# Performance work log

Hardware: AMD Instinct MI355X
Metric: run time of the kernel (lower is better)

Reference implementation:

```python
import jax, jax.numpy as jnp
import numpy as np

N = 50000   # nodes
E = 800000  # edges per layer
D = 128     # feature dim
H = 256     # mlp hidden
O = 3       # output dim


def setup_inputs() -> dict:
    key = jax.random.key(0)
    ks = jax.random.split(key, 16)
    def lin(k, fan_out, fan_in):
        s = 1.0 / np.sqrt(fan_in)
        kw, kb = jax.random.split(k)
        return (jax.random.uniform(kw, (fan_out, fan_in), jnp.float32, -s, s),
                jax.random.uniform(kb, (fan_out,), jnp.float32, -s, s))
    x = jax.random.normal(ks[0], (N, D), jnp.float32)
    edge_idx0 = jax.random.randint(ks[1], (2, E), 0, N, dtype=jnp.int64)
    edge_idx1 = jax.random.randint(ks[2], (2, E), 0, N, dtype=jnp.int64)
    Wl1, bl1 = lin(ks[3], D, D)   # SAGE layer1: lin_l (aggregated neighbors, with bias)
    Wr1, _ = lin(ks[4], D, D)     # SAGE layer1: lin_r (root, no bias)
    Wl2, bl2 = lin(ks[5], D, D)
    Wr2, _ = lin(ks[6], D, D)
    Ws, bs = lin(ks[7], D, D)     # skip_fc
    W1, b1 = lin(ks[8], H, D)     # mlp hidden
    W2, b2 = lin(ks[9], O, H)     # mlp out
    return dict(x=x, edge_idx0=edge_idx0, edge_idx1=edge_idx1,
                Wl1=Wl1, bl1=bl1, Wr1=Wr1, Wl2=Wl2, bl2=bl2, Wr2=Wr2,
                Ws=Ws, bs=bs, W1=W1, b1=b1, W2=W2, b2=b2)


def _sage(x, ei, Wl, bl, Wr):
    # PyG SAGEConv with mean aggregation: out = lin_l(mean_j x_j) + lin_r(x_i)
    src, dst = ei[0], ei[1]
    agg = jax.ops.segment_sum(x[src], dst, num_segments=N)          # [N, D] gather-scatter
    cnt = jax.ops.segment_sum(jnp.ones((ei.shape[1],), x.dtype), dst, num_segments=N)
    agg = agg / jnp.maximum(cnt, 1.0)[:, None]
    return agg @ Wl.T + bl + x @ Wr.T


def reference(x, edge_idx0, edge_idx1, Wl1, bl1, Wr1, Wl2, bl2, Wr2,
              Ws, bs, W1, b1, W2, b2):
    inp = x
    h = _sage(x, edge_idx0, Wl1, bl1, Wr1)
    h = _sage(h, edge_idx1, Wl2, bl2, Wr2)
    h = h + (inp @ Ws.T + bs)            # skip connection
    h = jax.nn.relu(h @ W1.T + b1)       # MLP head
    return h @ W2.T + b2                  # [N, 3]
```

## Files before the change

kernel.cpp:

```cpp
#include <hip/hip_runtime.h>
#include <hip/hip_bf16.h>


#define DD 128
#define SB 8
#define CH 4096
typedef unsigned short u16;
typedef __attribute__((ext_vector_type(8))) short short8;
typedef __attribute__((ext_vector_type(4))) float f32x4;

__device__ inline u16 f2bf(float f) {
    __hip_bfloat16 h = __float2bfloat16(f);
    u16 u;
    __builtin_memcpy(&u, &h, 2);
    return u;
}
__device__ inline unsigned pack2(float lo, float hi) {
    return (unsigned)f2bf(lo) | ((unsigned)f2bf(hi) << 16);
}
__device__ inline float bf_lo(unsigned u) { union { unsigned x; float f; } c; c.x = u << 16; return c.f; }
__device__ inline float bf_hi(unsigned u) { union { unsigned x; float f; } c; c.x = u & 0xffff0000u; return c.f; }

struct CastJobs {
    const float4* src[6];
    uint2* dst[6];
    int qstart[7];
};
__global__ __launch_bounds__(256) void cast_kernel(CastJobs jb) {
    int q = blockIdx.x * 256 + threadIdx.x;
    if (q >= jb.qstart[6]) return;
    int i = 0;
#pragma unroll
    for (int k = 1; k < 6; ++k) if (q >= jb.qstart[k]) i = k;
    int local = q - jb.qstart[i];
    float4 v = jb.src[i][local];
    jb.dst[i][local] = make_uint2(pack2(v.x, v.y), pack2(v.z, v.w));
}

__global__ __launch_bounds__(256) void hist1_kernel(const int* __restrict__ dst0, int* __restrict__ h0,
                                                    const int* __restrict__ dst1, int* __restrict__ h1,
                                                    int e0, int e1, int nb, int P) {
    int arr = blockIdx.y;
    const int* dst = arr ? dst1 : dst0;
    int* hist = arr ? h1 : h0;
    int e = arr ? e1 : e0;
    __shared__ int h[256];
    int t = threadIdx.x;
    h[t] = 0;
    __syncthreads();
    int base = blockIdx.x * CH;
    int hi = min(base + CH, e);
    for (int i = base + t; i < hi; i += 256) atomicAdd(&h[dst[i] >> SB], 1);
    __syncthreads();
    if (t < nb) hist[t * P + blockIdx.x] = h[t];
}

__global__ __launch_bounds__(256) void rowsum_kernel(const int* __restrict__ h0, int* __restrict__ bs0,
                                                     const int* __restrict__ h1, int* __restrict__ bs1,
                                                     int P) {
    int arr = blockIdx.y;
    const int* hist = arr ? h1 : h0;
    int* bs = arr ? bs1 : bs0;
    int b = blockIdx.x;
    __shared__ int s[256];
    int t = threadIdx.x;
    s[t] = (t < P) ? hist[b * P + t] : 0;
    __syncthreads();
    for (int off = 128; off; off >>= 1) {
        if (t < off) s[t] += s[t + off];
        __syncthreads();
    }
    if (t == 0) bs[b] = s[0];
}

__global__ __launch_bounds__(256) void bscan_kernel(const int* __restrict__ bs0, int* __restrict__ bb0, int* __restrict__ rp0, int e0,
                                                    const int* __restrict__ bs1, int* __restrict__ bb1, int* __restrict__ rp1, int e1,
                                                    int nb, int n) {
    int arr = blockIdx.x;
    const int* bsum = arr ? bs1 : bs0;
    int* bb = arr ? bb1 : bb0;
    int* rp = arr ? rp1 : rp0;
    int E = arr ? e1 : e0;
    __shared__ int s[256];
    int t = threadIdx.x;
    int v = (t < nb) ? bsum[t] : 0;
    s[t] = v;
    __syncthreads();
    for (int off = 1; off < 256; off <<= 1) {
        int u = (t >= off) ? s[t - off] : 0;
        __syncthreads();
        s[t] += u;
        __syncthreads();
    }
    if (t < nb) bb[t] = s[t] - v;
    if (t == 0) { bb[nb] = E; rp[n] = E; }
}

__global__ __launch_bounds__(256) void offs_kernel(int* __restrict__ h0, const int* __restrict__ bb0,
                                                   int* __restrict__ h1, const int* __restrict__ bb1,
                                                   int P) {
    int arr = blockIdx.y;
    int* hist = arr ? h1 : h0;
    const int* bb = arr ? bb1 : bb0;
    int b = blockIdx.x;
    __shared__ int s[256];
    int t = threadIdx.x;
    int v = (t < P) ? hist[b * P + t] : 0;
    s[t] = v;
    __syncthreads();
    for (int off = 1; off < 256; off <<= 1) {
        int u = (t >= off) ? s[t - off] : 0;
        __syncthreads();
        s[t] += u;
        __syncthreads();
    }
    if (t < P) hist[b * P + t] = s[t] - v + bb[b];
}

__global__ __launch_bounds__(256) void scatter1_kernel(
    const int* __restrict__ src0, const int* __restrict__ dst0, const int* __restrict__ h0, unsigned* __restrict__ binned0,
    const int* __restrict__ src1, const int* __restrict__ dst1, const int* __restrict__ h1, unsigned* __restrict__ binned1,
    int e0, int e1, int nb, int P) {
    int arr = blockIdx.y;
    const int* src = arr ? src1 : src0;
    const int* dst = arr ? dst1 : dst0;
    const int* hist = arr ? h1 : h0;
    unsigned* binned = arr ? binned1 : binned0;
    int e = arr ? e1 : e0;
    int p = blockIdx.x;
    __shared__ int cnt[256];
    int t = threadIdx.x;
    if (t < nb) cnt[t] = hist[t * P + p];
    __syncthreads();
    int base = p * CH;
    int hi = min(base + CH, e);
    for (int i = base + t; i < hi; i += 256) {
        int d = dst[i];
        int pos = atomicAdd(&cnt[d >> SB], 1);
        binned[pos] = ((unsigned)d << 16) | (unsigned)src[i];
    }
}

__global__ __launch_bounds__(256) void place_kernel(
    const unsigned* __restrict__ binned0, const int* __restrict__ bb0, int* __restrict__ rp0, u16* __restrict__ csr0,
    const unsigned* __restrict__ binned1, const int* __restrict__ bb1, int* __restrict__ rp1, u16* __restrict__ csr1,
    int n, int nb) {
    int arr = blockIdx.y;
    const unsigned* binned = arr ? binned1 : binned0;
    const int* bb = arr ? bb1 : bb0;
    int* rp = arr ? rp1 : rp0;
    u16* csr = arr ? csr1 : csr0;
    int b = blockIdx.x;
    __shared__ int cnt[256];
    __shared__ int s[256];
    int t = threadIdx.x;
    int base = bb[b], end = bb[b + 1];
    cnt[t] = 0;
    __syncthreads();
    for (int i = base + t; i < end; i += 256)
        atomicAdd(&cnt[(binned[i] >> 16) & 255], 1);
    __syncthreads();
    int deg = cnt[t];
    s[t] = deg;
    __syncthreads();
    for (int off = 1; off < 256; off <<= 1) {
        int u = (t >= off) ? s[t - off] : 0;
        __syncthreads();
        s[t] += u;
        __syncthreads();
    }
    int gpos = base + s[t] - deg;
    int node = (b << SB) + t;
    if (node < n) rp[node] = gpos;
    cnt[t] = gpos;
    __syncthreads();
    for (int i = base + t; i < end; i += 256) {
        unsigned pk = binned[i];
        int ld = (pk >> 16) & 255;
        int pos = atomicAdd(&cnt[ld], 1);
        csr[pos] = (u16)(pk & 0xffffu);
    }
}

__global__ __launch_bounds__(256) void agg1_kernel(const u16* __restrict__ G1,
                                                   const u16* __restrict__ csr,
                                                   const int* __restrict__ rp,
                                                   const float* __restrict__ bl1,
                                                   u16* __restrict__ h1, int n) {
    int g = (blockIdx.x * 256 + threadIdx.x) >> 4;
    int lane = threadIdx.x & 15;
    if (g >= n) return;
    int start = rp[g], end = rp[g + 1];
    int d = end - start;
    const uint4* X4 = (const uint4*)G1;
    float acc[8] = {0.f, 0.f, 0.f, 0.f, 0.f, 0.f, 0.f, 0.f};
    int e = start;
    for (; e + 3 < end; e += 4) {
        int s0 = csr[e], s1 = csr[e + 1], s2 = csr[e + 2], s3 = csr[e + 3];
        uint4 v0 = X4[(size_t)s0 * 48 + lane];
        uint4 v1 = X4[(size_t)s1 * 48 + lane];
        uint4 v2 = X4[(size_t)s2 * 48 + lane];
        uint4 v3 = X4[(size_t)s3 * 48 + lane];
        acc[0] += (bf_lo(v0.x) + bf_lo(v1.x)) + (bf_lo(v2.x) + bf_lo(v3.x));
        acc[1] += (bf_hi(v0.x) + bf_hi(v1.x)) + (bf_hi(v2.x) + bf_hi(v3.x));
        acc[2] += (bf_lo(v0.y) + bf_lo(v1.y)) + (bf_lo(v2.y) + bf_lo(v3.y));
        acc[3] += (bf_hi(v0.y) + bf_hi(v1.y)) + (bf_hi(v2.y) + bf_hi(v3.y));
        acc[4] += (bf_lo(v0.z) + bf_lo(v1.z)) + (bf_lo(v2.z) + bf_lo(v3.z));
        acc[5] += (bf_hi(v0.z) + bf_hi(v1.z)) + (bf_hi(v2.z) + bf_hi(v3.z));
        acc[6] += (bf_lo(v0.w) + bf_lo(v1.w)) + (bf_lo(v2.w) + bf_lo(v3.w));
        acc[7] += (bf_hi(v0.w) + bf_hi(v1.w)) + (bf_hi(v2.w) + bf_hi(v3.w));
    }
    for (; e < end; ++e) {
        uint4 v0 = X4[(size_t)csr[e] * 48 + lane];
        acc[0] += bf_lo(v0.x); acc[1] += bf_hi(v0.x);
        acc[2] += bf_lo(v0.y); acc[3] += bf_hi(v0.y);
        acc[4] += bf_lo(v0.z); acc[5] += bf_hi(v0.z);
        acc[6] += bf_lo(v0.w); acc[7] += bf_hi(v0.w);
    }
    float sc = 1.0f / (float)max(d, 1);
    uint4 m = X4[(size_t)g * 48 + 16 + lane];
    const float4* bl = (const float4*)bl1;
    float4 ba = bl[lane * 2], bb = bl[lane * 2 + 1];
    uint4 r;
    r.x = pack2(acc[0] * sc + bf_lo(m.x) + ba.x, acc[1] * sc + bf_hi(m.x) + ba.y);
    r.y = pack2(acc[2] * sc + bf_lo(m.y) + ba.z, acc[3] * sc + bf_hi(m.y) + ba.w);
    r.z = pack2(acc[4] * sc + bf_lo(m.z) + bb.x, acc[5] * sc + bf_hi(m.z) + bb.y);
    r.w = pack2(acc[6] * sc + bf_lo(m.w) + bb.z, acc[7] * sc + bf_hi(m.w) + bb.w);
    ((uint4*)h1)[(size_t)g * 16 + lane] = r;
}

__global__ __launch_bounds__(256) void agg2_kernel(const u16* __restrict__ G2,
                                                   const u16* __restrict__ G1,
                                                   const u16* __restrict__ csr,
                                                   const int* __restrict__ rp,
                                                   const float* __restrict__ bl2,
                                                   const float* __restrict__ bs,
                                                   u16* __restrict__ h3, int n) {
    int g = (blockIdx.x * 256 + threadIdx.x) >> 4;
    int lane = threadIdx.x & 15;
    if (g >= n) return;
    int start = rp[g], end = rp[g + 1];
    int d = end - start;
    const uint4* X4 = (const uint4*)G2;
    float acc[8] = {0.f, 0.f, 0.f, 0.f, 0.f, 0.f, 0.f, 0.f};
    int e = start;
    for (; e + 3 < end; e += 4) {
        int s0 = csr[e], s1 = csr[e + 1], s2 = csr[e + 2], s3 = csr[e + 3];
        uint4 v0 = X4[(size_t)s0 * 32 + lane];
        uint4 v1 = X4[(size_t)s1 * 32 + lane];
        uint4 v2 = X4[(size_t)s2 * 32 + lane];
        uint4 v3 = X4[(size_t)s3 * 32 + lane];
        acc[0] += (bf_lo(v0.x) + bf_lo(v1.x)) + (bf_lo(v2.x) + bf_lo(v3.x));
        acc[1] += (bf_hi(v0.x) + bf_hi(v1.x)) + (bf_hi(v2.x) + bf_hi(v3.x));
        acc[2] += (bf_lo(v0.y) + bf_lo(v1.y)) + (bf_lo(v2.y) + bf_lo(v3.y));
        acc[3] += (bf_hi(v0.y) + bf_hi(v1.y)) + (bf_hi(v2.y) + bf_hi(v3.y));
        acc[4] += (bf_lo(v0.z) + bf_lo(v1.z)) + (bf_lo(v2.z) + bf_lo(v3.z));
        acc[5] += (bf_hi(v0.z) + bf_hi(v1.z)) + (bf_hi(v2.z) + bf_hi(v3.z));
        acc[6] += (bf_lo(v0.w) + bf_lo(v1.w)) + (bf_lo(v2.w) + bf_lo(v3.w));
        acc[7] += (bf_hi(v0.w) + bf_hi(v1.w)) + (bf_hi(v2.w) + bf_hi(v3.w));
    }
    for (; e < end; ++e) {
        uint4 v0 = X4[(size_t)csr[e] * 32 + lane];
        acc[0] += bf_lo(v0.x); acc[1] += bf_hi(v0.x);
        acc[2] += bf_lo(v0.y); acc[3] += bf_hi(v0.y);
        acc[4] += bf_lo(v0.z); acc[5] += bf_hi(v0.z);
        acc[6] += bf_lo(v0.w); acc[7] += bf_hi(v0.w);
    }
    float sc = 1.0f / (float)max(d, 1);
    uint4 m2 = X4[(size_t)g * 32 + 16 + lane];
    uint4 m1 = ((const uint4*)G1)[(size_t)g * 48 + 32 + lane];
    const float4* c2 = (const float4*)bl2;
    const float4* cs = (const float4*)bs;
    float4 ba = c2[lane * 2], bb = c2[lane * 2 + 1];
    float4 sa = cs[lane * 2], sb = cs[lane * 2 + 1];
    uint4 r;
    r.x = pack2(acc[0] * sc + bf_lo(m2.x) + bf_lo(m1.x) + ba.x + sa.x,
                acc[1] * sc + bf_hi(m2.x) + bf_hi(m1.x) + ba.y + sa.y);
    r.y = pack2(acc[2] * sc + bf_lo(m2.y) + bf_lo(m1.y) + ba.z + sa.z,
                acc[3] * sc + bf_hi(m2.y) + bf_hi(m1.y) + ba.w + sa.w);
    r.z = pack2(acc[4] * sc + bf_lo(m2.z) + bf_lo(m1.z) + bb.x + sb.x,
                acc[5] * sc + bf_hi(m2.z) + bf_hi(m1.z) + bb.y + sb.y);
    r.w = pack2(acc[6] * sc + bf_lo(m2.w) + bf_lo(m1.w) + bb.z + sb.z,
                acc[7] * sc + bf_hi(m2.w) + bf_hi(m1.w) + bb.w + sb.w);
    ((uint4*)h3)[(size_t)g * 16 + lane] = r;
}

template <bool F32A>
__global__ __launch_bounds__(256) void mfma_gemm(const void* __restrict__ Av,
                                                 const u16* __restrict__ W,
                                                 u16* __restrict__ C, int M, int NC) {
    __shared__ u16 Bs[32 * 512];
    const int t = threadIdx.x;
    const int colBase = blockIdx.y * 128;
#pragma unroll
    for (int i = 0; i < 8; ++i) {
        int id = t + 256 * i;
        int nrow = id >> 4, cc = id & 15;
        int f = ((nrow >> 4) << 2) | (cc >> 2);
        int dl = ((cc & 3) << 4) | (nrow & 15);
        *(uint4*)&Bs[(f * 64 + dl) * 8] = ((const uint4*)W)[(size_t)(colBase + nrow) * 16 + cc];
    }
    __syncthreads();
    const int w = t >> 6, lane = t & 63, r = lane & 15, half = lane >> 4;
    const int nTiles = M >> 4;
    const int nWaves = gridDim.x * 4;
    const u16* bB = &Bs[lane * 8];
    for (int tile = blockIdx.x * 4 + w; tile < nTiles; tile += nWaves) {
        int rowA = (tile << 4) + r;
        short8 af[4];
        if (F32A) {
            const float4* Arow = (const float4*)Av + (size_t)rowA * 32 + half * 2;
#pragma unroll
            for (int kk = 0; kk < 4; ++kk) {
                float4 a = Arow[kk * 8], b = Arow[kk * 8 + 1];
                uint4 v = make_uint4(pack2(a.x, a.y), pack2(a.z, a.w),
                                     pack2(b.x, b.y), pack2(b.z, b.w));
                af[kk] = *(short8*)&v;
            }
        } else {
            const uint4* Arow = (const uint4*)Av + (size_t)rowA * 16 + half;
#pragma unroll
            for (int kk = 0; kk < 4; ++kk) {
                uint4 v = Arow[kk * 4];
                af[kk] = *(short8*)&v;
            }
        }
        f32x4 acc[8];
#pragma unroll
        for (int i = 0; i < 8; ++i) acc[i] = (f32x4){0.f, 0.f, 0.f, 0.f};
#pragma unroll
        for (int kk = 0; kk < 4; ++kk)
#pragma unroll
            for (int ct = 0; ct < 8; ++ct) {
                short8 bf = *(const short8*)(bB + (ct * 4 + kk) * 512);
                acc[ct] = __builtin_amdgcn_mfma_f32_16x16x32_bf16(af[kk], bf, acc[ct], 0, 0, 0);
            }
#pragma unroll
        for (int ct = 0; ct < 8; ++ct) {
            int col = colBase + ct * 16 + r;
#pragma unroll
            for (int reg = 0; reg < 4; ++reg) {
                int row = (tile << 4) + half * 4 + reg;
                C[(size_t)row * NC + col] = f2bf(acc[ct][reg]);
            }
        }
    }
}

__global__ __launch_bounds__(256) void gemm_out_kernel(const u16* __restrict__ h3,
                                                       const u16* __restrict__ W1,
                                                       const float* __restrict__ b1,
                                                       const float* __restrict__ W2,
                                                       const float* __restrict__ b2,
                                                       float* __restrict__ out, int M) {
    __shared__ u16 Bs[64 * 512];
    __shared__ float w2s[3 * 256];
    __shared__ float b1s[256];
    const int t = threadIdx.x;
#pragma unroll
    for (int i = 0; i < 16; ++i) {
        int id = t + 256 * i;
        int nrow = id >> 4, cc = id & 15;
        int f = ((nrow >> 4) << 2) | (cc >> 2);
        int dl = ((cc & 3) << 4) | (nrow & 15);
        *(uint4*)&Bs[(f * 64 + dl) * 8] = ((const uint4*)W1)[(size_t)nrow * 16 + cc];
    }
    for (int i = t; i < 768; i += 256) w2s[i] = W2[i];
    b1s[t] = b1[t];
    __syncthreads();
    const int w = t >> 6, lane = t & 63, r = lane & 15, half = lane >> 4;
    const int nTiles = M >> 4;
    const int nWaves = gridDim.x * 4;
    const u16* bB = &Bs[lane * 8];
    float c0 = b2[0], c1 = b2[1], c2 = b2[2];
    for (int tile = blockIdx.x * 4 + w; tile < nTiles; tile += nWaves) {
        int rowA = (tile << 4) + r;
        const uint4* Arow = (const uint4*)h3 + (size_t)rowA * 16 + half;
        short8 af[4];
#pragma unroll
        for (int kk = 0; kk < 4; ++kk) {
            uint4 v = Arow[kk * 4];
            af[kk] = *(short8*)&v;
        }
        f32x4 acc[16];
#pragma unroll
        for (int i = 0; i < 16; ++i) acc[i] = (f32x4){0.f, 0.f, 0.f, 0.f};
#pragma unroll
        for (int kk = 0; kk < 4; ++kk)
#pragma unroll
            for (int ct = 0; ct < 16; ++ct) {
                short8 bf = *(const short8*)(bB + (ct * 4 + kk) * 512);
                acc[ct] = __builtin_amdgcn_mfma_f32_16x16x32_bf16(af[kk], bf, acc[ct], 0, 0, 0);
            }
        float p[4][3] = {{0.f, 0.f, 0.f}, {0.f, 0.f, 0.f}, {0.f, 0.f, 0.f}, {0.f, 0.f, 0.f}};
#pragma unroll
        for (int ct = 0; ct < 16; ++ct) {
            int col = ct * 16 + r;
            float bv = b1s[col];
            float w0 = w2s[col], w1 = w2s[256 + col], w2v = w2s[512 + col];
#pragma unroll
            for (int reg = 0; reg < 4; ++reg) {
                float h4 = fmaxf(acc[ct][reg] + bv, 0.f);
                p[reg][0] += h4 * w0;
                p[reg][1] += h4 * w1;
                p[reg][2] += h4 * w2v;
            }
        }
#pragma unroll
        for (int m = 1; m < 16; m <<= 1)
#pragma unroll
            for (int reg = 0; reg < 4; ++reg) {
                p[reg][0] += __shfl_xor(p[reg][0], m);
                p[reg][1] += __shfl_xor(p[reg][1], m);
                p[reg][2] += __shfl_xor(p[reg][2], m);
            }
        if (r == 0) {
#pragma unroll
            for (int reg = 0; reg < 4; ++reg) {
                int row = (tile << 4) + half * 4 + reg;
                out[(size_t)row * 3 + 0] = p[reg][0] + c0;
                out[(size_t)row * 3 + 1] = p[reg][1] + c1;
                out[(size_t)row * 3 + 2] = p[reg][2] + c2;
            }
        }
    }
}

extern "C" void kernel_launch(void* const* d_in, const int* in_sizes, int n_in,
                              void* d_out, int out_size, void* d_ws, size_t ws_size,
                              hipStream_t stream) {
    const float* x   = (const float*)d_in[0];
    const int*   ei0 = (const int*)d_in[1];
    const int*   ei1 = (const int*)d_in[2];
    const float* Wl1 = (const float*)d_in[3];
    const float* bl1 = (const float*)d_in[4];
    const float* Wr1 = (const float*)d_in[5];
    const float* Wl2 = (const float*)d_in[6];
    const float* bl2 = (const float*)d_in[7];
    const float* Wr2 = (const float*)d_in[8];
    const float* Wsk = (const float*)d_in[9];
    const float* bsk = (const float*)d_in[10];
    const float* W1  = (const float*)d_in[11];
    const float* b1  = (const float*)d_in[12];
    const float* W2  = (const float*)d_in[13];
    const float* b2  = (const float*)d_in[14];
    float* out = (float*)d_out;

    const int N  = in_sizes[0] / DD;
    const int E0 = in_sizes[1] / 2;
    const int E1 = in_sizes[2] / 2;
    const int H  = in_sizes[12];

    const int* src0 = ei0;      const int* dst0 = ei0 + E0;
    const int* src1 = ei1;      const int* dst1 = ei1 + E1;

    const int nb   = (N + 255) >> SB;
    const int Emax = (E0 > E1) ? E0 : E1;
    const int P    = (Emax + CH - 1) / CH;

    char* wp = (char*)d_ws;
    auto carve = [&](size_t bytes) { char* p = wp; wp += (bytes + 255) & ~(size_t)255; return p; };
    u16* G1   = (u16*)carve((size_t)N * 384 * 2);
    u16* G2   = (u16*)carve((size_t)N * 256 * 2);
    u16* h1h  = (u16*)carve((size_t)N * DD * 2);
    u16* h3h  = (u16*)carve((size_t)N * DD * 2);
    u16* wc1  = (u16*)carve((size_t)384 * DD * 2);
    u16* wc2  = (u16*)carve((size_t)256 * DD * 2);
    u16* w1h  = (u16*)carve((size_t)H * DD * 2);
    int* rp0  = (int*)carve((size_t)(N + 1) * 4);
    int* rp1  = (int*)carve((size_t)(N + 1) * 4);
    u16* csr0 = (u16*)carve((size_t)E0 * 2);
    u16* csr1 = (u16*)carve((size_t)E1 * 2);
    unsigned* binned0 = (unsigned*)carve((size_t)E0 * 4);
    unsigned* binned1 = (unsigned*)carve((size_t)E1 * 4);
    int* hist1_0 = (int*)carve((size_t)nb * P * 4);
    int* hist1_1 = (int*)carve((size_t)nb * P * 4);
    int* bsum0 = (int*)carve((size_t)nb * 4);
    int* bsum1 = (int*)carve((size_t)nb * 4);
    int* bb0 = (int*)carve((size_t)(nb + 1) * 4);
    int* bb1 = (int*)carve((size_t)(nb + 1) * 4);

    CastJobs jb;
    const float* srcs[6] = {Wl1, Wr1, Wsk, Wl2, Wr2, W1};
    u16* dsts[6] = {wc1, wc1 + 128 * DD, wc1 + 256 * DD, wc2, wc2 + 128 * DD, w1h};
    int  cnts[6] = {DD * DD, DD * DD, DD * DD, DD * DD, DD * DD, H * DD};
    int q = 0;
    for (int i = 0; i < 6; ++i) {
        jb.src[i] = (const float4*)srcs[i];
        jb.dst[i] = (uint2*)dsts[i];
        jb.qstart[i] = q;
        q += cnts[i] / 4;
    }
    jb.qstart[6] = q;

    const int gAgg = (N * 16 + 255) / 256;

    cast_kernel<<<(q + 255) / 256, 256, 0, stream>>>(jb);
    hist1_kernel<<<dim3(P, 2), 256, 0, stream>>>(dst0, hist1_0, dst1, hist1_1, E0, E1, nb, P);
    rowsum_kernel<<<dim3(nb, 2), 256, 0, stream>>>(hist1_0, bsum0, hist1_1, bsum1, P);
    bscan_kernel<<<2, 256, 0, stream>>>(bsum0, bb0, rp0, E0, bsum1, bb1, rp1, E1, nb, N);
    offs_kernel<<<dim3(nb, 2), 256, 0, stream>>>(hist1_0, bb0, hist1_1, bb1, P);
    scatter1_kernel<<<dim3(P, 2), 256, 0, stream>>>(src0, dst0, hist1_0, binned0,
                                                    src1, dst1, hist1_1, binned1, E0, E1, nb, P);
    place_kernel<<<dim3(nb, 2), 256, 0, stream>>>(binned0, bb0, rp0, csr0,
                                                  binned1, bb1, rp1, csr1, N, nb);

    mfma_gemm<true><<<dim3(320, 3), 256, 0, stream>>>(x, wc1, G1, N, 384);
    agg1_kernel<<<gAgg, 256, 0, stream>>>(G1, csr0, rp0, bl1, h1h, N);
    mfma_gemm<false><<<dim3(320, 2), 256, 0, stream>>>(h1h, wc2, G2, N, 256);
    agg2_kernel<<<gAgg, 256, 0, stream>>>(G2, G1, csr1, rp1, bl2, bsk, h3h, N);
    gemm_out_kernel<<<512, 256, 0, stream>>>(h3h, w1h, b1, W2, b2, out, N);
}
```

Baseline: 257.6 us.

## Fuse neighbor aggregation into following MFMA GEMMs and enlarge edge chunk size

The separate mean-aggregation kernels are removed. Aggregation for layer one now runs inside the layer-two GEMM, and aggregation for layer two inside the output MLP kernel. Each wave gathers the neighbor rows for its 16-row tile directly into MFMA A-fragments, which removes the h1/h3 intermediate writes and reads and two launches. The trade-off is that gathers become per-row and serialised across degree within a wave, with divergent loop lengths among the 16 rows of a tile, and only 512 blocks are launched. The edge chunk size for the binning passes is also doubled.

```diff
diff --git a/kernel.cpp b/kernel.cpp
--- a/kernel.cpp
+++ b/kernel.cpp
@@ -4,7 +4,7 @@
 
 #define DD 128
 #define SB 8
-#define CH 4096
+#define CH 8192
 typedef unsigned short u16;
 typedef __attribute__((ext_vector_type(8))) short short8;
 typedef __attribute__((ext_vector_type(4))) float f32x4;
@@ -182,109 +182,6 @@
     }
 }
 
-__global__ __launch_bounds__(256) void agg1_kernel(const u16* __restrict__ G1,
-                                                   const u16* __restrict__ csr,
-                                                   const int* __restrict__ rp,
-                                                   const float* __restrict__ bl1,
-                                                   u16* __restrict__ h1, int n) {
-    int g = (blockIdx.x * 256 + threadIdx.x) >> 4;
-    int lane = threadIdx.x & 15;
-    if (g >= n) return;
-    int start = rp[g], end = rp[g + 1];
-    int d = end - start;
-    const uint4* X4 = (const uint4*)G1;
-    float acc[8] = {0.f, 0.f, 0.f, 0.f, 0.f, 0.f, 0.f, 0.f};
-    int e = start;
-    for (; e + 3 < end; e += 4) {
-        int s0 = csr[e], s1 = csr[e + 1], s2 = csr[e + 2], s3 = csr[e + 3];
-        uint4 v0 = X4[(size_t)s0 * 48 + lane];
-        uint4 v1 = X4[(size_t)s1 * 48 + lane];
-        uint4 v2 = X4[(size_t)s2 * 48 + lane];
-        uint4 v3 = X4[(size_t)s3 * 48 + lane];
-        acc[0] += (bf_lo(v0.x) + bf_lo(v1.x)) + (bf_lo(v2.x) + bf_lo(v3.x));
-        acc[1] += (bf_hi(v0.x) + bf_hi(v1.x)) + (bf_hi(v2.x) + bf_hi(v3.x));
-        acc[2] += (bf_lo(v0.y) + bf_lo(v1.y)) + (bf_lo(v2.y) + bf_lo(v3.y));
-        acc[3] += (bf_hi(v0.y) + bf_hi(v1.y)) + (bf_hi(v2.y) + bf_hi(v3.y));
-        acc[4] += (bf_lo(v0.z) + bf_lo(v1.z)) + (bf_lo(v2.z) + bf_lo(v3.z));
-        acc[5] += (bf_hi(v0.z) + bf_hi(v1.z)) + (bf_hi(v2.z) + bf_hi(v3.z));
-        acc[6] += (bf_lo(v0.w) + bf_lo(v1.w)) + (bf_lo(v2.w) + bf_lo(v3.w));
-        acc[7] += (bf_hi(v0.w) + bf_hi(v1.w)) + (bf_hi(v2.w) + bf_hi(v3.w));
-    }
-    for (; e < end; ++e) {
-        uint4 v0 = X4[(size_t)csr[e] * 48 + lane];
-        acc[0] += bf_lo(v0.x); acc[1] += bf_hi(v0.x);
-        acc[2] += bf_lo(v0.y); acc[3] += bf_hi(v0.y);
-        acc[4] += bf_lo(v0.z); acc[5] += bf_hi(v0.z);
-        acc[6] += bf_lo(v0.w); acc[7] += bf_hi(v0.w);
-    }
-    float sc = 1.0f / (float)max(d, 1);
-    uint4 m = X4[(size_t)g * 48 + 16 + lane];
-    const float4* bl = (const float4*)bl1;
-    float4 ba = bl[lane * 2], bb = bl[lane * 2 + 1];
-    uint4 r;
-    r.x = pack2(acc[0] * sc + bf_lo(m.x) + ba.x, acc[1] * sc + bf_hi(m.x) + ba.y);
-    r.y = pack2(acc[2] * sc + bf_lo(m.y) + ba.z, acc[3] * sc + bf_hi(m.y) + ba.w);
-    r.z = pack2(acc[4] * sc + bf_lo(m.z) + bb.x, acc[5] * sc + bf_hi(m.z) + bb.y);
-    r.w = pack2(acc[6] * sc + bf_lo(m.w) + bb.z, acc[7] * sc + bf_hi(m.w) + bb.w);
-    ((uint4*)h1)[(size_t)g * 16 + lane] = r;
-}
-
-__global__ __launch_bounds__(256) void agg2_kernel(const u16* __restrict__ G2,
-                                                   const u16* __restrict__ G1,
-                                                   const u16* __restrict__ csr,
-                                                   const int* __restrict__ rp,
-                                                   const float* __restrict__ bl2,
-                                                   const float* __restrict__ bs,
-                                                   u16* __restrict__ h3, int n) {
-    int g = (blockIdx.x * 256 + threadIdx.x) >> 4;
-    int lane = threadIdx.x & 15;
-    if (g >= n) return;
-    int start = rp[g], end = rp[g + 1];
-    int d = end - start;
-    const uint4* X4 = (const uint4*)G2;
-    float acc[8] = {0.f, 0.f, 0.f, 0.f, 0.f, 0.f, 0.f, 0.f};
-    int e = start;
-    for (; e + 3 < end; e += 4) {
-        int s0 = csr[e], s1 = csr[e + 1], s2 = csr[e + 2], s3 = csr[e + 3];
-        uint4 v0 = X4[(size_t)s0 * 32 + lane];
-        uint4 v1 = X4[(size_t)s1 * 32 + lane];
-        uint4 v2 = X4[(size_t)s2 * 32 + lane];
-        uint4 v3 = X4[(size_t)s3 * 32 + lane];
-        acc[0] += (bf_lo(v0.x) + bf_lo(v1.x)) + (bf_lo(v2.x) + bf_lo(v3.x));
-        acc[1] += (bf_hi(v0.x) + bf_hi(v1.x)) + (bf_hi(v2.x) + bf_hi(v3.x));
-        acc[2] += (bf_lo(v0.y) + bf_lo(v1.y)) + (bf_lo(v2.y) + bf_lo(v3.y));
-        acc[3] += (bf_hi(v0.y) + bf_hi(v1.y)) + (bf_hi(v2.y) + bf_hi(v3.y));
-        acc[4] += (bf_lo(v0.z) + bf_lo(v1.z)) + (bf_lo(v2.z) + bf_lo(v3.z));
-        acc[5] += (bf_hi(v0.z) + bf_hi(v1.z)) + (bf_hi(v2.z) + bf_hi(v3.z));
-        acc[6] += (bf_lo(v0.w) + bf_lo(v1.w)) + (bf_lo(v2.w) + bf_lo(v3.w));
-        acc[7] += (bf_hi(v0.w) + bf_hi(v1.w)) + (bf_hi(v2.w) + bf_hi(v3.w));
-    }
-    for (; e < end; ++e) {
-        uint4 v0 = X4[(size_t)csr[e] * 32 + lane];
-        acc[0] += bf_lo(v0.x); acc[1] += bf_hi(v0.x);
-        acc[2] += bf_lo(v0.y); acc[3] += bf_hi(v0.y);
-        acc[4] += bf_lo(v0.z); acc[5] += bf_hi(v0.z);
-        acc[6] += bf_lo(v0.w); acc[7] += bf_hi(v0.w);
-    }
-    float sc = 1.0f / (float)max(d, 1);
-    uint4 m2 = X4[(size_t)g * 32 + 16 + lane];
-    uint4 m1 = ((const uint4*)G1)[(size_t)g * 48 + 32 + lane];
-    const float4* c2 = (const float4*)bl2;
-    const float4* cs = (const float4*)bs;
-    float4 ba = c2[lane * 2], bb = c2[lane * 2 + 1];
-    float4 sa = cs[lane * 2], sb = cs[lane * 2 + 1];
-    uint4 r;
-    r.x = pack2(acc[0] * sc + bf_lo(m2.x) + bf_lo(m1.x) + ba.x + sa.x,
-                acc[1] * sc + bf_hi(m2.x) + bf_hi(m1.x) + ba.y + sa.y);
-    r.y = pack2(acc[2] * sc + bf_lo(m2.y) + bf_lo(m1.y) + ba.z + sa.z,
-                acc[3] * sc + bf_hi(m2.y) + bf_hi(m1.y) + ba.w + sa.w);
-    r.z = pack2(acc[4] * sc + bf_lo(m2.z) + bf_lo(m1.z) + bb.x + sb.x,
-                acc[5] * sc + bf_hi(m2.z) + bf_hi(m1.z) + bb.y + sb.y);
-    r.w = pack2(acc[6] * sc + bf_lo(m2.w) + bf_lo(m1.w) + bb.z + sb.z,
-                acc[7] * sc + bf_hi(m2.w) + bf_hi(m1.w) + bb.w + sb.w);
-    ((uint4*)h3)[(size_t)g * 16 + lane] = r;
-}
-
 template <bool F32A>
 __global__ __launch_bounds__(256) void mfma_gemm(const void* __restrict__ Av,
                                                  const u16* __restrict__ W,
@@ -347,15 +244,111 @@
     }
 }
 
-__global__ __launch_bounds__(256) void gemm_out_kernel(const u16* __restrict__ h3,
-                                                       const u16* __restrict__ W1,
-                                                       const float* __restrict__ b1,
-                                                       const float* __restrict__ W2,
-                                                       const float* __restrict__ b2,
-                                                       float* __restrict__ out, int M) {
+__global__ __launch_bounds__(256) void g2_fused_kernel(const u16* __restrict__ G1,
+                                                       const u16* __restrict__ csr,
+                                                       const int* __restrict__ rp,
+                                                       const float* __restrict__ bl1,
+                                                       const u16* __restrict__ W,
+                                                       u16* __restrict__ G2, int M) {
     __shared__ u16 Bs[64 * 512];
-    __shared__ float w2s[3 * 256];
+    __shared__ float bls[128];
+    const int t = threadIdx.x;
+#pragma unroll
+    for (int i = 0; i < 16; ++i) {
+        int id = t + 256 * i;
+        int nrow = id >> 4, cc = id & 15;
+        int f = ((nrow >> 4) << 2) | (cc >> 2);
+        int dl = ((cc & 3) << 4) | (nrow & 15);
+        *(uint4*)&Bs[(f * 64 + dl) * 8] = ((const uint4*)W)[(size_t)nrow * 16 + cc];
+    }
+    if (t < 128) bls[t] = bl1[t];
+    __syncthreads();
+    const int w = t >> 6, lane = t & 63, r = lane & 15, half = lane >> 4;
+    const int nTiles = M >> 4;
+    const uint4* G14 = (const uint4*)G1;
+    const u16* bB = &Bs[lane * 8];
+    for (int tile = blockIdx.x * 4 + w; tile < nTiles; tile += gridDim.x * 4) {
+        int row = (tile << 4) + r;
+        int start = rp[row], end = rp[row + 1];
+        float acc[4][8];
+#pragma unroll
+        for (int kk = 0; kk < 4; ++kk)
+#pragma unroll
+            for (int j = 0; j < 8; ++j) acc[kk][j] = 0.f;
+        int e = start;
+        for (; e + 1 < end; e += 2) {
+            int s0 = csr[e], s1 = csr[e + 1];
+#pragma unroll
+            for (int kk = 0; kk < 4; ++kk) {
+                uint4 v0 = G14[(size_t)s0 * 48 + kk * 4 + half];
+                uint4 v1 = G14[(size_t)s1 * 48 + kk * 4 + half];
+                acc[kk][0] += bf_lo(v0.x) + bf_lo(v1.x); acc[kk][1] += bf_hi(v0.x) + bf_hi(v1.x);
+                acc[kk][2] += bf_lo(v0.y) + bf_lo(v1.y); acc[kk][3] += bf_hi(v0.y) + bf_hi(v1.y);
+                acc[kk][4] += bf_lo(v0.z) + bf_lo(v1.z); acc[kk][5] += bf_hi(v0.z) + bf_hi(v1.z);
+                acc[kk][6] += bf_lo(v0.w) + bf_lo(v1.w); acc[kk][7] += bf_hi(v0.w) + bf_hi(v1.w);
+            }
+        }
+        if (e < end) {
+            int s0 = csr[e];
+#pragma unroll
+            for (int kk = 0; kk < 4; ++kk) {
+                uint4 v0 = G14[(size_t)s0 * 48 + kk * 4 + half];
+                acc[kk][0] += bf_lo(v0.x); acc[kk][1] += bf_hi(v0.x);
+                acc[kk][2] += bf_lo(v0.y); acc[kk][3] += bf_hi(v0.y);
+                acc[kk][4] += bf_lo(v0.z); acc[kk][5] += bf_hi(v0.z);
+                acc[kk][6] += bf_lo(v0.w); acc[kk][7] += bf_hi(v0.w);
+            }
+        }
+        float sc = 1.0f / (float)max(end - start, 1);
+        short8 af[4];
+#pragma unroll
+        for (int kk = 0; kk < 4; ++kk) {
+            uint4 m = G14[(size_t)row * 48 + 16 + kk * 4 + half];
+            const float* bp = &bls[half * 8 + kk * 32];
+            uint4 vv;
+            vv.x = pack2(acc[kk][0] * sc + bf_lo(m.x) + bp[0], acc[kk][1] * sc + bf_hi(m.x) + bp[1]);
+            vv.y = pack2(acc[kk][2] * sc + bf_lo(m.y) + bp[2], acc[kk][3] * sc + bf_hi(m.y) + bp[3]);
+            vv.z = pack2(acc[kk][4] * sc + bf_lo(m.z) + bp[4], acc[kk][5] * sc + bf_hi(m.z) + bp[5]);
+            vv.w = pack2(acc[kk][6] * sc + bf_lo(m.w) + bp[6], acc[kk][7] * sc + bf_hi(m.w) + bp[7]);
+            af[kk] = *(short8*)&vv;
+        }
+        f32x4 C[16];
+#pragma unroll
+        for (int i = 0; i < 16; ++i) C[i] = (f32x4){0.f, 0.f, 0.f, 0.f};
+#pragma unroll
+        for (int kk = 0; kk < 4; ++kk)
+#pragma unroll
+            for (int ct = 0; ct < 16; ++ct) {
+                short8 bf = *(const short8*)(bB + (ct * 4 + kk) * 512);
+                C[ct] = __builtin_amdgcn_mfma_f32_16x16x32_bf16(af[kk], bf, C[ct], 0, 0, 0);
+            }
+#pragma unroll
+        for (int ct = 0; ct < 16; ++ct) {
+            int col = ct * 16 + r;
+#pragma unroll
+            for (int reg = 0; reg < 4; ++reg) {
+                int orow = (tile << 4) + half * 4 + reg;
+                G2[(size_t)orow * 256 + col] = f2bf(C[ct][reg]);
+            }
+        }
+    }
+}
+
+__global__ __launch_bounds__(256) void out_fused_kernel(const u16* __restrict__ G2,
+                                                        const u16* __restrict__ G1,
+                                                        const u16* __restrict__ csr,
+                                                        const int* __restrict__ rp,
+                                                        const float* __restrict__ bl2,
+                                                        const float* __restrict__ bsk,
+                                                        const u16* __restrict__ W1,
+                                                        const float* __restrict__ b1,
+                                                        const float* __restrict__ W2,
+                                                        const float* __restrict__ b2,
+                                                        float* __restrict__ out, int M) {
+    __shared__ u16 Bs[64 * 512];
+    __shared__ float w2s[768];
     __shared__ float b1s[256];
+    __shared__ float bls[128];
     const int t = threadIdx.x;
 #pragma unroll
     for (int i = 0; i < 16; ++i) {
@@ -367,30 +360,73 @@
     }
     for (int i = t; i < 768; i += 256) w2s[i] = W2[i];
     b1s[t] = b1[t];
+    if (t < 128) bls[t] = bl2[t] + bsk[t];
     __syncthreads();
     const int w = t >> 6, lane = t & 63, r = lane & 15, half = lane >> 4;
     const int nTiles = M >> 4;
-    const int nWaves = gridDim.x * 4;
+    const uint4* G24 = (const uint4*)G2;
+    const uint4* G14 = (const uint4*)G1;
     const u16* bB = &Bs[lane * 8];
     float c0 = b2[0], c1 = b2[1], c2 = b2[2];
-    for (int tile = blockIdx.x * 4 + w; tile < nTiles; tile += nWaves) {
-        int rowA = (tile << 4) + r;
-        const uint4* Arow = (const uint4*)h3 + (size_t)rowA * 16 + half;
+    for (int tile = blockIdx.x * 4 + w; tile < nTiles; tile += gridDim.x * 4) {
+        int row = (tile << 4) + r;
+        int start = rp[row], end = rp[row + 1];
+        float acc[4][8];
+#pragma unroll
+        for (int kk = 0; kk < 4; ++kk)
+#pragma unroll
+            for (int j = 0; j < 8; ++j) acc[kk][j] = 0.f;
+        int e = start;
+        for (; e + 1 < end; e += 2) {
+            int s0 = csr[e], s1 = csr[e + 1];
+#pragma unroll
+            for (int kk = 0; kk < 4; ++kk) {
+                uint4 v0 = G24[(size_t)s0 * 32 + kk * 4 + half];
+                uint4 v1 = G24[(size_t)s1 * 32 + kk * 4 + half];
+                acc[kk][0] += bf_lo(v0.x) + bf_lo(v1.x); acc[kk][1] += bf_hi(v0.x) + bf_hi(v1.x);
+                acc[kk][2] += bf_lo(v0.y) + bf_lo(v1.y); acc[kk][3] += bf_hi(v0.y) + bf_hi(v1.y);
+                acc[kk][4] += bf_lo(v0.z) + bf_lo(v1.z); acc[kk][5] += bf_hi(v0.z) + bf_hi(v1.z);
+                acc[kk][6] += bf_lo(v0.w) + bf_lo(v1.w); acc[kk][7] += bf_hi(v0.w) + bf_hi(v1.w);
+            }
+        }
+        if (e < end) {
+            int s0 = csr[e];
+#pragma unroll
+            for (int kk = 0; kk < 4; ++kk) {
+                uint4 v0 = G24[(size_t)s0 * 32 + kk * 4 + half];
+                acc[kk][0] += bf_lo(v0.x); acc[kk][1] += bf_hi(v0.x);
+                acc[kk][2] += bf_lo(v0.y); acc[kk][3] += bf_hi(v0.y);
+                acc[kk][4] += bf_lo(v0.z); acc[kk][5] += bf_hi(v0.z);
+                acc[kk][6] += bf_lo(v0.w); acc[kk][7] += bf_hi(v0.w);
+            }
+        }
+        float sc = 1.0f / (float)max(end - start, 1);
         short8 af[4];
 #pragma unroll
         for (int kk = 0; kk < 4; ++kk) {
-            uint4 v = Arow[kk * 4];
-            af[kk] = *(short8*)&v;
-        }
-        f32x4 acc[16];
-#pragma unroll
-        for (int i = 0; i < 16; ++i) acc[i] = (f32x4){0.f, 0.f, 0.f, 0.f};
+            uint4 m2 = G24[(size_t)row * 32 + 16 + kk * 4 + half];
+            uint4 m1 = G14[(size_t)row * 48 + 32 + kk * 4 + half];
+            const float* bp = &bls[half * 8 + kk * 32];
+            uint4 vv;
+            vv.x = pack2(acc[kk][0] * sc + bf_lo(m2.x) + bf_lo(m1.x) + bp[0],
+                         acc[kk][1] * sc + bf_hi(m2.x) + bf_hi(m1.x) + bp[1]);
+            vv.y = pack2(acc[kk][2] * sc + bf_lo(m2.y) + bf_lo(m1.y) + bp[2],
+                         acc[kk][3] * sc + bf_hi(m2.y) + bf_hi(m1.y) + bp[3]);
+            vv.z = pack2(acc[kk][4] * sc + bf_lo(m2.z) + bf_lo(m1.z) + bp[4],
+                         acc[kk][5] * sc + bf_hi(m2.z) + bf_hi(m1.z) + bp[5]);
+            vv.w = pack2(acc[kk][6] * sc + bf_lo(m2.w) + bf_lo(m1.w) + bp[6],
+                         acc[kk][7] * sc + bf_hi(m2.w) + bf_hi(m1.w) + bp[7]);
+            af[kk] = *(short8*)&vv;
+        }
+        f32x4 C[16];
+#pragma unroll
+        for (int i = 0; i < 16; ++i) C[i] = (f32x4){0.f, 0.f, 0.f, 0.f};
 #pragma unroll
         for (int kk = 0; kk < 4; ++kk)
 #pragma unroll
             for (int ct = 0; ct < 16; ++ct) {
                 short8 bf = *(const short8*)(bB + (ct * 4 + kk) * 512);
-                acc[ct] = __builtin_amdgcn_mfma_f32_16x16x32_bf16(af[kk], bf, acc[ct], 0, 0, 0);
+                C[ct] = __builtin_amdgcn_mfma_f32_16x16x32_bf16(af[kk], bf, C[ct], 0, 0, 0);
             }
         float p[4][3] = {{0.f, 0.f, 0.f}, {0.f, 0.f, 0.f}, {0.f, 0.f, 0.f}, {0.f, 0.f, 0.f}};
 #pragma unroll
@@ -400,7 +436,7 @@
             float w0 = w2s[col], w1 = w2s[256 + col], w2v = w2s[512 + col];
 #pragma unroll
             for (int reg = 0; reg < 4; ++reg) {
-                float h4 = fmaxf(acc[ct][reg] + bv, 0.f);
+                float h4 = fmaxf(C[ct][reg] + bv, 0.f);
                 p[reg][0] += h4 * w0;
                 p[reg][1] += h4 * w1;
                 p[reg][2] += h4 * w2v;
@@ -417,10 +453,10 @@
         if (r == 0) {
 #pragma unroll
             for (int reg = 0; reg < 4; ++reg) {
-                int row = (tile << 4) + half * 4 + reg;
-                out[(size_t)row * 3 + 0] = p[reg][0] + c0;
-                out[(size_t)row * 3 + 1] = p[reg][1] + c1;
-                out[(size_t)row * 3 + 2] = p[reg][2] + c2;
+                int orow = (tile << 4) + half * 4 + reg;
+                out[(size_t)orow * 3 + 0] = p[reg][0] + c0;
+                out[(size_t)orow * 3 + 1] = p[reg][1] + c1;
+                out[(size_t)orow * 3 + 2] = p[reg][2] + c2;
             }
         }
     }
@@ -462,8 +498,6 @@
     auto carve = [&](size_t bytes) { char* p = wp; wp += (bytes + 255) & ~(size_t)255; return p; };
     u16* G1   = (u16*)carve((size_t)N * 384 * 2);
     u16* G2   = (u16*)carve((size_t)N * 256 * 2);
-    u16* h1h  = (u16*)carve((size_t)N * DD * 2);
-    u16* h3h  = (u16*)carve((size_t)N * DD * 2);
     u16* wc1  = (u16*)carve((size_t)384 * DD * 2);
     u16* wc2  = (u16*)carve((size_t)256 * DD * 2);
     u16* w1h  = (u16*)carve((size_t)H * DD * 2);
@@ -493,8 +527,6 @@
     }
     jb.qstart[6] = q;
 
-    const int gAgg = (N * 16 + 255) / 256;
-
     cast_kernel<<<(q + 255) / 256, 256, 0, stream>>>(jb);
     hist1_kernel<<<dim3(P, 2), 256, 0, stream>>>(dst0, hist1_0, dst1, hist1_1, E0, E1, nb, P);
     rowsum_kernel<<<dim3(nb, 2), 256, 0, stream>>>(hist1_0, bsum0, hist1_1, bsum1, P);
@@ -506,8 +538,7 @@
                                                   binned1, bb1, rp1, csr1, N, nb);
 
     mfma_gemm<true><<<dim3(320, 3), 256, 0, stream>>>(x, wc1, G1, N, 384);
-    agg1_kernel<<<gAgg, 256, 0, stream>>>(G1, csr0, rp0, bl1, h1h, N);
-    mfma_gemm<false><<<dim3(320, 2), 256, 0, stream>>>(h1h, wc2, G2, N, 256);
-    agg2_kernel<<<gAgg, 256, 0, stream>>>(G2, G1, csr1, rp1, bl2, bsk, h3h, N);
-    gemm_out_kernel<<<512, 256, 0, stream>>>(h3h, w1h, b1, W2, b2, out, N);
-}
+    g2_fused_kernel<<<512, 256, 0, stream>>>(G1, csr0, rp0, bl1, wc2, G2, N);
+    out_fused_kernel<<<512, 256, 0, stream>>>(G2, G1, csr1, rp1, bl2, bsk,
+                                              w1h, b1, W2, b2, out, N);
+}
```

New measurement: 381.0 us. 47.9% more time.

## Split projected feature buffers into planar blocks and fold rowsum into scan

Applied to the files above, without the earlier changes.

The GEMM outputs G1 and G2 are now stored as separate contiguous N×128 planes (lin_l, lin_r, skip) rather than interleaved rows of 384 or 256 columns. This lets the gather in the aggregation kernels touch a dense 25.6MB-class table, so cache lines and L2 residency are spent only on the gathered projection. The rowsum kernel is removed: the scan kernel now sums histogram rows serially per thread. The histogram chunk size is doubled so there are half as many partitions, which keeps that serial loop short but gives fewer blocks in the hist and scatter passes.

```diff
diff --git a/kernel.cpp b/kernel.cpp
--- a/kernel.cpp
+++ b/kernel.cpp
@@ -4,7 +4,7 @@
 
 #define DD 128
 #define SB 8
-#define CH 4096
+#define CH 8192
 typedef unsigned short u16;
 typedef __attribute__((ext_vector_type(8))) short short8;
 typedef __attribute__((ext_vector_type(4))) float f32x4;
@@ -55,35 +55,21 @@
     if (t < nb) hist[t * P + blockIdx.x] = h[t];
 }
 
-__global__ __launch_bounds__(256) void rowsum_kernel(const int* __restrict__ h0, int* __restrict__ bs0,
-                                                     const int* __restrict__ h1, int* __restrict__ bs1,
-                                                     int P) {
-    int arr = blockIdx.y;
+__global__ __launch_bounds__(256) void bscan_kernel(const int* __restrict__ h0, int* __restrict__ bb0, int* __restrict__ rp0, int e0,
+                                                    const int* __restrict__ h1, int* __restrict__ bb1, int* __restrict__ rp1, int e1,
+                                                    int nb, int P, int n) {
+    int arr = blockIdx.x;
     const int* hist = arr ? h1 : h0;
-    int* bs = arr ? bs1 : bs0;
-    int b = blockIdx.x;
-    __shared__ int s[256];
-    int t = threadIdx.x;
-    s[t] = (t < P) ? hist[b * P + t] : 0;
-    __syncthreads();
-    for (int off = 128; off; off >>= 1) {
-        if (t < off) s[t] += s[t + off];
-        __syncthreads();
-    }
-    if (t == 0) bs[b] = s[0];
-}
-
-__global__ __launch_bounds__(256) void bscan_kernel(const int* __restrict__ bs0, int* __restrict__ bb0, int* __restrict__ rp0, int e0,
-                                                    const int* __restrict__ bs1, int* __restrict__ bb1, int* __restrict__ rp1, int e1,
-                                                    int nb, int n) {
-    int arr = blockIdx.x;
-    const int* bsum = arr ? bs1 : bs0;
     int* bb = arr ? bb1 : bb0;
     int* rp = arr ? rp1 : rp0;
     int E = arr ? e1 : e0;
     __shared__ int s[256];
     int t = threadIdx.x;
-    int v = (t < nb) ? bsum[t] : 0;
+    int v = 0;
+    if (t < nb) {
+        const int* row = hist + (size_t)t * P;
+        for (int p = 0; p < P; ++p) v += row[p];
+    }
     s[t] = v;
     __syncthreads();
     for (int off = 1; off < 256; off <<= 1) {
@@ -182,7 +168,8 @@
     }
 }
 
-__global__ __launch_bounds__(256) void agg1_kernel(const u16* __restrict__ G1,
+__global__ __launch_bounds__(256) void agg1_kernel(const uint4* __restrict__ G1L,
+                                                   const uint4* __restrict__ G1M,
                                                    const u16* __restrict__ csr,
                                                    const int* __restrict__ rp,
                                                    const float* __restrict__ bl1,
@@ -192,15 +179,14 @@
     if (g >= n) return;
     int start = rp[g], end = rp[g + 1];
     int d = end - start;
-    const uint4* X4 = (const uint4*)G1;
     float acc[8] = {0.f, 0.f, 0.f, 0.f, 0.f, 0.f, 0.f, 0.f};
     int e = start;
     for (; e + 3 < end; e += 4) {
         int s0 = csr[e], s1 = csr[e + 1], s2 = csr[e + 2], s3 = csr[e + 3];
-        uint4 v0 = X4[(size_t)s0 * 48 + lane];
-        uint4 v1 = X4[(size_t)s1 * 48 + lane];
-        uint4 v2 = X4[(size_t)s2 * 48 + lane];
-        uint4 v3 = X4[(size_t)s3 * 48 + lane];
+        uint4 v0 = G1L[(size_t)s0 * 16 + lane];
+        uint4 v1 = G1L[(size_t)s1 * 16 + lane];
+        uint4 v2 = G1L[(size_t)s2 * 16 + lane];
+        uint4 v3 = G1L[(size_t)s3 * 16 + lane];
         acc[0] += (bf_lo(v0.x) + bf_lo(v1.x)) + (bf_lo(v2.x) + bf_lo(v3.x));
         acc[1] += (bf_hi(v0.x) + bf_hi(v1.x)) + (bf_hi(v2.x) + bf_hi(v3.x));
         acc[2] += (bf_lo(v0.y) + bf_lo(v1.y)) + (bf_lo(v2.y) + bf_lo(v3.y));
@@ -211,14 +197,14 @@
         acc[7] += (bf_hi(v0.w) + bf_hi(v1.w)) + (bf_hi(v2.w) + bf_hi(v3.w));
     }
     for (; e < end; ++e) {
-        uint4 v0 = X4[(size_t)csr[e] * 48 + lane];
+        uint4 v0 = G1L[(size_t)csr[e] * 16 + lane];
         acc[0] += bf_lo(v0.x); acc[1] += bf_hi(v0.x);
         acc[2] += bf_lo(v0.y); acc[3] += bf_hi(v0.y);
         acc[4] += bf_lo(v0.z); acc[5] += bf_hi(v0.z);
         acc[6] += bf_lo(v0.w); acc[7] += bf_hi(v0.w);
     }
     float sc = 1.0f / (float)max(d, 1);
-    uint4 m = X4[(size_t)g * 48 + 16 + lane];
+    uint4 m = G1M[(size_t)g * 16 + lane];
     const float4* bl = (const float4*)bl1;
     float4 ba = bl[lane * 2], bb = bl[lane * 2 + 1];
     uint4 r;
@@ -229,8 +215,9 @@
     ((uint4*)h1)[(size_t)g * 16 + lane] = r;
 }
 
-__global__ __launch_bounds__(256) void agg2_kernel(const u16* __restrict__ G2,
-                                                   const u16* __restrict__ G1,
+__global__ __launch_bounds__(256) void agg2_kernel(const uint4* __restrict__ G2L,
+                                                   const uint4* __restrict__ G2R,
+                                                   const uint4* __restrict__ G1R,
                                                    const u16* __restrict__ csr,
                                                    const int* __restrict__ rp,
                                                    const float* __restrict__ bl2,
@@ -241,15 +228,14 @@
     if (g >= n) return;
     int start = rp[g], end = rp[g + 1];
     int d = end - start;
-    const uint4* X4 = (const uint4*)G2;
     float acc[8] = {0.f, 0.f, 0.f, 0.f, 0.f, 0.f, 0.f, 0.f};
     int e = start;
     for (; e + 3 < end; e += 4) {
         int s0 = csr[e], s1 = csr[e + 1], s2 = csr[e + 2], s3 = csr[e + 3];
-        uint4 v0 = X4[(size_t)s0 * 32 + lane];
-        uint4 v1 = X4[(size_t)s1 * 32 + lane];
-        uint4 v2 = X4[(size_t)s2 * 32 + lane];
-        uint4 v3 = X4[(size_t)s3 * 32 + lane];
+        uint4 v0 = G2L[(size_t)s0 * 16 + lane];
+        uint4 v1 = G2L[(size_t)s1 * 16 + lane];
+        uint4 v2 = G2L[(size_t)s2 * 16 + lane];
+        uint4 v3 = G2L[(size_t)s3 * 16 + lane];
         acc[0] += (bf_lo(v0.x) + bf_lo(v1.x)) + (bf_lo(v2.x) + bf_lo(v3.x));
         acc[1] += (bf_hi(v0.x) + bf_hi(v1.x)) + (bf_hi(v2.x) + bf_hi(v3.x));
         acc[2] += (bf_lo(v0.y) + bf_lo(v1.y)) + (bf_lo(v2.y) + bf_lo(v3.y));
@@ -260,15 +246,15 @@
         acc[7] += (bf_hi(v0.w) + bf_hi(v1.w)) + (bf_hi(v2.w) + bf_hi(v3.w));
     }
     for (; e < end; ++e) {
-        uint4 v0 = X4[(size_t)csr[e] * 32 + lane];
+        uint4 v0 = G2L[(size_t)csr[e] * 16 + lane];
         acc[0] += bf_lo(v0.x); acc[1] += bf_hi(v0.x);
         acc[2] += bf_lo(v0.y); acc[3] += bf_hi(v0.y);
         acc[4] += bf_lo(v0.z); acc[5] += bf_hi(v0.z);
         acc[6] += bf_lo(v0.w); acc[7] += bf_hi(v0.w);
     }
     float sc = 1.0f / (float)max(d, 1);
-    uint4 m2 = X4[(size_t)g * 32 + 16 + lane];
-    uint4 m1 = ((const uint4*)G1)[(size_t)g * 48 + 32 + lane];
+    uint4 m2 = G2R[(size_t)g * 16 + lane];
+    uint4 m1 = G1R[(size_t)g * 16 + lane];
     const float4* c2 = (const float4*)bl2;
     const float4* cs = (const float4*)bs;
     float4 ba = c2[lane * 2], bb = c2[lane * 2 + 1];
@@ -288,10 +274,11 @@
 template <bool F32A>
 __global__ __launch_bounds__(256) void mfma_gemm(const void* __restrict__ Av,
                                                  const u16* __restrict__ W,
-                                                 u16* __restrict__ C, int M, int NC) {
+                                                 u16* __restrict__ C, int M) {
     __shared__ u16 Bs[32 * 512];
     const int t = threadIdx.x;
     const int colBase = blockIdx.y * 128;
+    u16* Cp = C + (size_t)blockIdx.y * M * 128;
 #pragma unroll
     for (int i = 0; i < 8; ++i) {
         int id = t + 256 * i;
@@ -337,11 +324,11 @@
             }
 #pragma unroll
         for (int ct = 0; ct < 8; ++ct) {
-            int col = colBase + ct * 16 + r;
+            int col = ct * 16 + r;
 #pragma unroll
             for (int reg = 0; reg < 4; ++reg) {
                 int row = (tile << 4) + half * 4 + reg;
-                C[(size_t)row * NC + col] = f2bf(acc[ct][reg]);
+                Cp[(size_t)row * 128 + col] = f2bf(acc[ct][reg]);
             }
         }
     }
@@ -460,8 +447,8 @@
 
     char* wp = (char*)d_ws;
     auto carve = [&](size_t bytes) { char* p = wp; wp += (bytes + 255) & ~(size_t)255; return p; };
-    u16* G1   = (u16*)carve((size_t)N * 384 * 2);
-    u16* G2   = (u16*)carve((size_t)N * 256 * 2);
+    u16* G1   = (u16*)carve((size_t)3 * N * DD * 2);
+    u16* G2   = (u16*)carve((size_t)2 * N * DD * 2);
     u16* h1h  = (u16*)carve((size_t)N * DD * 2);
     u16* h3h  = (u16*)carve((size_t)N * DD * 2);
     u16* wc1  = (u16*)carve((size_t)384 * DD * 2);
@@ -475,10 +462,14 @@
     unsigned* binned1 = (unsigned*)carve((size_t)E1 * 4);
     int* hist1_0 = (int*)carve((size_t)nb * P * 4);
     int* hist1_1 = (int*)carve((size_t)nb * P * 4);
-    int* bsum0 = (int*)carve((size_t)nb * 4);
-    int* bsum1 = (int*)carve((size_t)nb * 4);
     int* bb0 = (int*)carve((size_t)(nb + 1) * 4);
     int* bb1 = (int*)carve((size_t)(nb + 1) * 4);
+
+    const u16* G1L = G1;
+    const u16* G1M = G1 + (size_t)N * DD;
+    const u16* G1R = G1 + (size_t)2 * N * DD;
+    const u16* G2L = G2;
+    const u16* G2R = G2 + (size_t)N * DD;
 
     CastJobs jb;
     const float* srcs[6] = {Wl1, Wr1, Wsk, Wl2, Wr2, W1};
@@ -497,17 +488,18 @@
 
     cast_kernel<<<(q + 255) / 256, 256, 0, stream>>>(jb);
     hist1_kernel<<<dim3(P, 2), 256, 0, stream>>>(dst0, hist1_0, dst1, hist1_1, E0, E1, nb, P);
-    rowsum_kernel<<<dim3(nb, 2), 256, 0, stream>>>(hist1_0, bsum0, hist1_1, bsum1, P);
-    bscan_kernel<<<2, 256, 0, stream>>>(bsum0, bb0, rp0, E0, bsum1, bb1, rp1, E1, nb, N);
+    bscan_kernel<<<2, 256, 0, stream>>>(hist1_0, bb0, rp0, E0, hist1_1, bb1, rp1, E1, nb, P, N);
     offs_kernel<<<dim3(nb, 2), 256, 0, stream>>>(hist1_0, bb0, hist1_1, bb1, P);
     scatter1_kernel<<<dim3(P, 2), 256, 0, stream>>>(src0, dst0, hist1_0, binned0,
                                                     src1, dst1, hist1_1, binned1, E0, E1, nb, P);
     place_kernel<<<dim3(nb, 2), 256, 0, stream>>>(binned0, bb0, rp0, csr0,
                                                   binned1, bb1, rp1, csr1, N, nb);
 
-    mfma_gemm<true><<<dim3(320, 3), 256, 0, stream>>>(x, wc1, G1, N, 384);
-    agg1_kernel<<<gAgg, 256, 0, stream>>>(G1, csr0, rp0, bl1, h1h, N);
-    mfma_gemm<false><<<dim3(320, 2), 256, 0, stream>>>(h1h, wc2, G2, N, 256);
-    agg2_kernel<<<gAgg, 256, 0, stream>>>(G2, G1, csr1, rp1, bl2, bsk, h3h, N);
+    mfma_gemm<true><<<dim3(320, 3), 256, 0, stream>>>(x, wc1, G1, N);
+    agg1_kernel<<<gAgg, 256, 0, stream>>>((const uint4*)G1L, (const uint4*)G1M,
+                                          csr0, rp0, bl1, h1h, N);
+    mfma_gemm<false><<<dim3(320, 2), 256, 0, stream>>>(h1h, wc2, G2, N);
+    agg2_kernel<<<gAgg, 256, 0, stream>>>((const uint4*)G2L, (const uint4*)G2R,
+                                          (const uint4*)G1R, csr1, rp1, bl2, bsk, h3h, N);
     gemm_out_kernel<<<512, 256, 0, stream>>>(h3h, w1h, b1, W2, b2, out, N);
 }
```

Result: slower. 272.2 us (+5.7%).
